# Performance work log

Hardware: AMD Instinct MI355X
Metric: run time of the kernel (lower is better)

The kernel has to match this reference:

```python
import jax, jax.numpy as jnp
import numpy as np

B, E, H, TOP_K = 4096, 64, 512, 8
NEG_INF = jnp.finfo(jnp.float32).min


def setup_inputs() -> dict:
    key = jax.random.key(0)
    ks = jax.random.split(key, 10)
    inv = lambda fan_in: 1.0 / np.sqrt(fan_in)
    return {
        "x_context": jax.random.normal(ks[0], (B, 68), dtype=jnp.float32),
        "x_q_values": jax.random.normal(ks[1], (B, E, 3), dtype=jnp.float32),
        "x_reward": jax.random.normal(ks[2], (B, E, 2), dtype=jnp.float32),
        "x_risk": jax.random.normal(ks[3], (B, E, 2), dtype=jnp.float32),
        # context_encoder: Linear(68, H)
        "Wc": jax.random.uniform(ks[4], (68, H), jnp.float32, -inv(68), inv(68)),
        "bc": jax.random.uniform(ks[5], (H,), jnp.float32, -inv(68), inv(68)),
        # expert_encoder: Linear(7, H)
        "We": jax.random.uniform(ks[6], (7, H), jnp.float32, -inv(7), inv(7)),
        "be": jax.random.uniform(ks[7], (H,), jnp.float32, -inv(7), inv(7)),
        # router_scorer: Linear(2H, 1)
        "Ws": jax.random.uniform(ks[8], (2 * H,), jnp.float32, -inv(2 * H), inv(2 * H)),
        "bs": jax.random.uniform(ks[9], (), jnp.float32, -inv(2 * H), inv(2 * H)),
    }


def reference(x_context, x_q_values, x_reward, x_risk, Wc, bc, We, be, Ws, bs):
    # context encoder: [B,68] -> [B,H]
    context_encoded = x_context @ Wc + bc
    # per-expert inputs: concat(q, reward, risk) -> [B,E,7] -> [B,E,H]
    expert_inputs = jnp.concatenate([x_q_values, x_reward, x_risk], axis=-1)
    expert_encoded = jnp.einsum("bef,fh->beh", expert_inputs, We) + be
    # scorer over concat([expert_encoded, context_expanded]): split the dot
    # product instead of materializing combined [B,E,2H] twice
    Ws_e, Ws_c = Ws[:H], Ws[H:]
    expert_logits = (
        jnp.einsum("beh,h->be", expert_encoded, Ws_e)
        + (context_encoded @ Ws_c)[:, None]
        + bs
    )  # [B,E]
    # top-k masked softmax
    topk_val, topk_idx = jax.lax.top_k(expert_logits, TOP_K)
    rows = jnp.arange(expert_logits.shape[0])[:, None]
    sparse = jnp.full_like(expert_logits, NEG_INF).at[rows, topk_idx].set(topk_val)
    gate_weights = jax.nn.softmax(sparse, axis=-1)  # [B,E]
    # gating bmm: [B,1,E] @ [B,E,3] -> [B,3]
    action_logits = jnp.einsum("be,bea->ba", gate_weights, x_q_values)
    return (action_logits, gate_weights, expert_logits)
```

## Files before the change

kernel.cpp:

```cpp
#include <hip/hip_runtime.h>
#include <cfloat>

#define NB 4096
#define NE 64
#define NH 512
#define TOPK 8
#define GRID 512
#define ROWS_PER_BLOCK (NB / GRID)

__global__ __launch_bounds__(256) void moe_router_fused(
    const float* __restrict__ x_context,
    const float* __restrict__ x_q,
    const float* __restrict__ x_r,
    const float* __restrict__ x_k,
    const float* __restrict__ Wc,
    const float* __restrict__ bc,
    const float* __restrict__ We,
    const float* __restrict__ be,
    const float* __restrict__ Ws,
    const float* __restrict__ bs,
    float* __restrict__ out_action,
    float* __restrict__ out_gate,
    float* __restrict__ out_logits)
{
    __shared__ float scoef[76];
    __shared__ __align__(16) float sval[4][64];

    int t = threadIdx.x;

    if (t < 76) {
        float acc = 0.f;
        if (t < 7) {
            const float4* row = (const float4*)(We + t * NH);
            const float4* wv  = (const float4*)(Ws);
            #pragma unroll 8
            for (int i = 0; i < NH / 4; ++i) {
                float4 a = row[i], b = wv[i];
                acc += a.x*b.x + a.y*b.y + a.z*b.z + a.w*b.w;
            }
        } else if (t < 75) {
            const float4* row = (const float4*)(Wc + (size_t)(t - 7) * NH);
            const float4* wv  = (const float4*)(Ws + NH);
            #pragma unroll 8
            for (int i = 0; i < NH / 4; ++i) {
                float4 a = row[i], b = wv[i];
                acc += a.x*b.x + a.y*b.y + a.z*b.z + a.w*b.w;
            }
        } else {
            const float4* b4  = (const float4*)be;
            const float4* c4  = (const float4*)bc;
            const float4* we4 = (const float4*)Ws;
            const float4* wc4 = (const float4*)(Ws + NH);
            #pragma unroll 8
            for (int i = 0; i < NH / 4; ++i) {
                float4 a = b4[i], w0 = we4[i], c = c4[i], w1 = wc4[i];
                acc += a.x*w0.x + a.y*w0.y + a.z*w0.z + a.w*w0.w
                     + c.x*w1.x + c.y*w1.y + c.z*w1.z + c.w*w1.w;
            }
            acc += bs[0];
        }
        scoef[t] = acc;
    }
    __syncthreads();

    int lane = t & 63;
    int w    = t >> 6;
    float* sc = sval[w];

    int b0 = blockIdx.x * ROWS_PER_BLOCK;
    #pragma unroll
    for (int it = 0; it < ROWS_PER_BLOCK / 4; ++it) {
        int b = b0 + it * 4 + w;

        const float* xc = x_context + (size_t)b * 68;
        float cb = xc[lane] * scoef[7 + lane];
        if (lane < 4) cb += xc[64 + lane] * scoef[71 + lane];
        #pragma unroll
        for (int off = 32; off; off >>= 1) cb += __shfl_xor(cb, off);

        size_t be_idx = (size_t)b * NE + lane;
        float q0 = x_q[be_idx * 3 + 0];
        float q1 = x_q[be_idx * 3 + 1];
        float q2 = x_q[be_idx * 3 + 2];
        float r0 = x_r[be_idx * 2 + 0];
        float r1 = x_r[be_idx * 2 + 1];
        float k0 = x_k[be_idx * 2 + 0];
        float k1 = x_k[be_idx * 2 + 1];

        float logit = q0 * scoef[0] + q1 * scoef[1] + q2 * scoef[2]
                    + r0 * scoef[3] + r1 * scoef[4]
                    + k0 * scoef[5] + k1 * scoef[6]
                    + scoef[75] + cb;

        out_logits[be_idx] = logit;

        sc[lane] = logit;
        float m = -FLT_MAX;
        int rank = 0;
        #pragma unroll
        for (int j = 0; j < 64; j += 4) {
            float4 v = *(const float4*)(sc + j);
            rank += (v.x > logit || (v.x == logit && (j + 0) < lane)) ? 1 : 0;
            rank += (v.y > logit || (v.y == logit && (j + 1) < lane)) ? 1 : 0;
            rank += (v.z > logit || (v.z == logit && (j + 2) < lane)) ? 1 : 0;
            rank += (v.w > logit || (v.w == logit && (j + 3) < lane)) ? 1 : 0;
            m = fmaxf(m, fmaxf(fmaxf(v.x, v.y), fmaxf(v.z, v.w)));
        }

        float e = (rank < TOPK) ? __expf(logit - m) : 0.f;
        float d  = e;
        float a0 = e * q0, a1 = e * q1, a2 = e * q2;
        #pragma unroll
        for (int off = 32; off; off >>= 1) {
            d  += __shfl_xor(d,  off);
            a0 += __shfl_xor(a0, off);
            a1 += __shfl_xor(a1, off);
            a2 += __shfl_xor(a2, off);
        }
        out_gate[be_idx] = e / d;
        if (lane == 0) {
            float inv = 1.f / d;
            out_action[(size_t)b * 3 + 0] = a0 * inv;
            out_action[(size_t)b * 3 + 1] = a1 * inv;
            out_action[(size_t)b * 3 + 2] = a2 * inv;
        }
    }
}

extern "C" void kernel_launch(void* const* d_in, const int* in_sizes, int n_in,
                              void* d_out, int out_size, void* d_ws, size_t ws_size,
                              hipStream_t stream) {
    const float* x_context = (const float*)d_in[0];
    const float* x_q       = (const float*)d_in[1];
    const float* x_r       = (const float*)d_in[2];
    const float* x_k       = (const float*)d_in[3];
    const float* Wc        = (const float*)d_in[4];
    const float* bc        = (const float*)d_in[5];
    const float* We        = (const float*)d_in[6];
    const float* be        = (const float*)d_in[7];
    const float* Ws        = (const float*)d_in[8];
    const float* bs        = (const float*)d_in[9];

    float* out        = (float*)d_out;
    float* out_action = out;
    float* out_gate   = out + NB * 3;
    float* out_logits = out + NB * 3 + NB * NE;

    moe_router_fused<<<GRID, 256, 0, stream>>>(
        x_context, x_q, x_r, x_k, Wc, bc, We, be, Ws, bs,
        out_action, out_gate, out_logits);
}
```

Baseline: 104.3 us.

## Split weight-folding precompute into separate kernel and use one row per wave

```diff
diff --git a/kernel.cpp b/kernel.cpp
--- a/kernel.cpp
+++ b/kernel.cpp
@@ -5,125 +5,107 @@
 #define NE 64
 #define NH 512
 #define TOPK 8
-#define GRID 512
-#define ROWS_PER_BLOCK (NB / GRID)
 
-__global__ __launch_bounds__(256) void moe_router_fused(
+__global__ void precompute_kernel(const float* __restrict__ Wc,
+                                  const float* __restrict__ bc,
+                                  const float* __restrict__ We,
+                                  const float* __restrict__ be,
+                                  const float* __restrict__ Ws,
+                                  const float* __restrict__ bs,
+                                  float* __restrict__ ws) {
+    int r = blockIdx.x;
+    int lane = threadIdx.x;
+    float partial = 0.f;
+    if (r < 7) {
+        const float* row = We + r * NH;
+        for (int h = lane; h < NH; h += 64) partial += row[h] * Ws[h];
+    } else if (r < 75) {
+        const float* row = Wc + (size_t)(r - 7) * NH;
+        for (int h = lane; h < NH; h += 64) partial += row[h] * Ws[NH + h];
+    } else {
+        for (int h = lane; h < NH; h += 64)
+            partial += be[h] * Ws[h] + bc[h] * Ws[NH + h];
+    }
+    #pragma unroll
+    for (int off = 32; off; off >>= 1) partial += __shfl_xor(partial, off);
+    if (lane == 0) {
+        if (r == 75) partial += bs[0];
+        ws[r] = partial;
+    }
+}
+
+__global__ __launch_bounds__(256) void router_kernel(
     const float* __restrict__ x_context,
     const float* __restrict__ x_q,
     const float* __restrict__ x_r,
     const float* __restrict__ x_k,
-    const float* __restrict__ Wc,
-    const float* __restrict__ bc,
-    const float* __restrict__ We,
-    const float* __restrict__ be,
-    const float* __restrict__ Ws,
-    const float* __restrict__ bs,
+    const float* __restrict__ ws,
     float* __restrict__ out_action,
     float* __restrict__ out_gate,
     float* __restrict__ out_logits)
 {
     __shared__ float scoef[76];
     __shared__ __align__(16) float sval[4][64];
-
     int t = threadIdx.x;
-
-    if (t < 76) {
-        float acc = 0.f;
-        if (t < 7) {
-            const float4* row = (const float4*)(We + t * NH);
-            const float4* wv  = (const float4*)(Ws);
-            #pragma unroll 8
-            for (int i = 0; i < NH / 4; ++i) {
-                float4 a = row[i], b = wv[i];
-                acc += a.x*b.x + a.y*b.y + a.z*b.z + a.w*b.w;
-            }
-        } else if (t < 75) {
-            const float4* row = (const float4*)(Wc + (size_t)(t - 7) * NH);
-            const float4* wv  = (const float4*)(Ws + NH);
-            #pragma unroll 8
-            for (int i = 0; i < NH / 4; ++i) {
-                float4 a = row[i], b = wv[i];
-                acc += a.x*b.x + a.y*b.y + a.z*b.z + a.w*b.w;
-            }
-        } else {
-            const float4* b4  = (const float4*)be;
-            const float4* c4  = (const float4*)bc;
-            const float4* we4 = (const float4*)Ws;
-            const float4* wc4 = (const float4*)(Ws + NH);
-            #pragma unroll 8
-            for (int i = 0; i < NH / 4; ++i) {
-                float4 a = b4[i], w0 = we4[i], c = c4[i], w1 = wc4[i];
-                acc += a.x*w0.x + a.y*w0.y + a.z*w0.z + a.w*w0.w
-                     + c.x*w1.x + c.y*w1.y + c.z*w1.z + c.w*w1.w;
-            }
-            acc += bs[0];
-        }
-        scoef[t] = acc;
-    }
+    if (t < 76) scoef[t] = ws[t];
     __syncthreads();
 
     int lane = t & 63;
-    int w    = t >> 6;
+    int w = t >> 6;
     float* sc = sval[w];
+    int b = blockIdx.x * 4 + w;
 
-    int b0 = blockIdx.x * ROWS_PER_BLOCK;
+    const float* xc = x_context + (size_t)b * 68;
+    float cb = xc[lane] * scoef[7 + lane];
+    if (lane < 4) cb += xc[64 + lane] * scoef[71 + lane];
     #pragma unroll
-    for (int it = 0; it < ROWS_PER_BLOCK / 4; ++it) {
-        int b = b0 + it * 4 + w;
+    for (int off = 32; off; off >>= 1) cb += __shfl_xor(cb, off);
 
-        const float* xc = x_context + (size_t)b * 68;
-        float cb = xc[lane] * scoef[7 + lane];
-        if (lane < 4) cb += xc[64 + lane] * scoef[71 + lane];
-        #pragma unroll
-        for (int off = 32; off; off >>= 1) cb += __shfl_xor(cb, off);
+    size_t be_idx = (size_t)b * NE + lane;
+    float q0 = x_q[be_idx * 3 + 0];
+    float q1 = x_q[be_idx * 3 + 1];
+    float q2 = x_q[be_idx * 3 + 2];
+    float r0 = x_r[be_idx * 2 + 0];
+    float r1 = x_r[be_idx * 2 + 1];
+    float k0 = x_k[be_idx * 2 + 0];
+    float k1 = x_k[be_idx * 2 + 1];
 
-        size_t be_idx = (size_t)b * NE + lane;
-        float q0 = x_q[be_idx * 3 + 0];
-        float q1 = x_q[be_idx * 3 + 1];
-        float q2 = x_q[be_idx * 3 + 2];
-        float r0 = x_r[be_idx * 2 + 0];
-        float r1 = x_r[be_idx * 2 + 1];
-        float k0 = x_k[be_idx * 2 + 0];
-        float k1 = x_k[be_idx * 2 + 1];
+    float logit = q0 * scoef[0] + q1 * scoef[1] + q2 * scoef[2]
+                + r0 * scoef[3] + r1 * scoef[4]
+                + k0 * scoef[5] + k1 * scoef[6]
+                + scoef[75] + cb;
 
-        float logit = q0 * scoef[0] + q1 * scoef[1] + q2 * scoef[2]
-                    + r0 * scoef[3] + r1 * scoef[4]
-                    + k0 * scoef[5] + k1 * scoef[6]
-                    + scoef[75] + cb;
+    out_logits[be_idx] = logit;
 
-        out_logits[be_idx] = logit;
+    sc[lane] = logit;
+    float m = -FLT_MAX;
+    int rank = 0;
+    #pragma unroll
+    for (int j = 0; j < 64; j += 4) {
+        float4 v = *(const float4*)(sc + j);
+        rank += (v.x > logit || (v.x == logit && (j + 0) < lane)) ? 1 : 0;
+        rank += (v.y > logit || (v.y == logit && (j + 1) < lane)) ? 1 : 0;
+        rank += (v.z > logit || (v.z == logit && (j + 2) < lane)) ? 1 : 0;
+        rank += (v.w > logit || (v.w == logit && (j + 3) < lane)) ? 1 : 0;
+        m = fmaxf(m, fmaxf(fmaxf(v.x, v.y), fmaxf(v.z, v.w)));
+    }
 
-        sc[lane] = logit;
-        float m = -FLT_MAX;
-        int rank = 0;
-        #pragma unroll
-        for (int j = 0; j < 64; j += 4) {
-            float4 v = *(const float4*)(sc + j);
-            rank += (v.x > logit || (v.x == logit && (j + 0) < lane)) ? 1 : 0;
-            rank += (v.y > logit || (v.y == logit && (j + 1) < lane)) ? 1 : 0;
-            rank += (v.z > logit || (v.z == logit && (j + 2) < lane)) ? 1 : 0;
-            rank += (v.w > logit || (v.w == logit && (j + 3) < lane)) ? 1 : 0;
-            m = fmaxf(m, fmaxf(fmaxf(v.x, v.y), fmaxf(v.z, v.w)));
-        }
-
-        float e = (rank < TOPK) ? __expf(logit - m) : 0.f;
-        float d  = e;
-        float a0 = e * q0, a1 = e * q1, a2 = e * q2;
-        #pragma unroll
-        for (int off = 32; off; off >>= 1) {
-            d  += __shfl_xor(d,  off);
-            a0 += __shfl_xor(a0, off);
-            a1 += __shfl_xor(a1, off);
-            a2 += __shfl_xor(a2, off);
-        }
-        out_gate[be_idx] = e / d;
-        if (lane == 0) {
-            float inv = 1.f / d;
-            out_action[(size_t)b * 3 + 0] = a0 * inv;
-            out_action[(size_t)b * 3 + 1] = a1 * inv;
-            out_action[(size_t)b * 3 + 2] = a2 * inv;
-        }
+    float e = (rank < TOPK) ? __expf(logit - m) : 0.f;
+    float d  = e;
+    float a0 = e * q0, a1 = e * q1, a2 = e * q2;
+    #pragma unroll
+    for (int off = 32; off; off >>= 1) {
+        d  += __shfl_xor(d,  off);
+        a0 += __shfl_xor(a0, off);
+        a1 += __shfl_xor(a1, off);
+        a2 += __shfl_xor(a2, off);
+    }
+    out_gate[be_idx] = e / d;
+    if (lane == 0) {
+        float inv = 1.f / d;
+        out_action[(size_t)b * 3 + 0] = a0 * inv;
+        out_action[(size_t)b * 3 + 1] = a1 * inv;
+        out_action[(size_t)b * 3 + 2] = a2 * inv;
     }
 }
 
@@ -145,8 +127,9 @@
     float* out_action = out;
     float* out_gate   = out + NB * 3;
     float* out_logits = out + NB * 3 + NB * NE;
+    float* wsf = (float*)d_ws;
 
-    moe_router_fused<<<GRID, 256, 0, stream>>>(
-        x_context, x_q, x_r, x_k, Wc, bc, We, be, Ws, bs,
-        out_action, out_gate, out_logits);
+    precompute_kernel<<<76, 64, 0, stream>>>(Wc, bc, We, be, Ws, bs, wsf);
+    router_kernel<<<NB / 4, 256, 0, stream>>>(x_context, x_q, x_r, x_k, wsf,
+                                              out_action, out_gate, out_logits);
 }
```

Measured after the change: 84.58 us. 1.23x faster.
